# Performance work log

Measured on AMD Instinct MI355X. Metric: run time of the kernel, lower is better.

Reference implementation:

```python
import jax, jax.numpy as jnp
import numpy as np

L = 64          # lattice side
NSITES = L * L  # 4096
HALF = NSITES // 2
B = 16384
H = 128         # hidden width of s/t MLPs
SLOPE = 0.2     # tf.nn.leaky_relu default alpha

# checkerboard parity indices (static, evenodd = 0)
_coords = np.arange(NSITES)
_parity = (_coords // L + _coords % L) % 2
IDX_A = jnp.asarray(np.where(_parity == 0)[0], dtype=jnp.int32)  # [HALF]
IDX_B = jnp.asarray(np.where(_parity == 1)[0], dtype=jnp.int32)  # [HALF]


def setup_inputs() -> dict:
    key = jax.random.key(0)
    ks = jax.random.split(key, 8)
    scale = 0.05  # small init keeps exp(-s) well-behaved
    return {
        "z":    jax.random.normal(ks[0], (B, NSITES), dtype=jnp.float32),
        "s_W0": jax.random.normal(ks[1], (HALF, H), dtype=jnp.float32) * scale,
        "s_W1": jax.random.normal(ks[2], (H, H), dtype=jnp.float32) * scale,
        "s_W2": jax.random.normal(ks[3], (H, HALF), dtype=jnp.float32) * scale,
        "s_b2": jnp.zeros((HALF,), dtype=jnp.float32),
        "t_W0": jax.random.normal(ks[4], (HALF, H), dtype=jnp.float32) * scale,
        "t_W1": jax.random.normal(ks[5], (H, H), dtype=jnp.float32) * scale,
        "t_W2": jax.random.normal(ks[6], (H, HALF), dtype=jnp.float32) * scale,
        "t_b2": jnp.zeros((HALF,), dtype=jnp.float32),
    }


def _mlp(x, W0, W1, W2, b2):
    # Dense(no bias)+leaky_relu x2, then Dense(with bias), matching the keras stack
    h = jax.nn.leaky_relu(x @ W0, negative_slope=SLOPE)
    h = jax.nn.leaky_relu(h @ W1, negative_slope=SLOPE)
    return h @ W2 + b2


def reference(z, s_W0, s_W1, s_W2, s_b2, t_W0, t_W1, t_W2, t_b2):
    z_a = z[:, IDX_A]                       # [B, HALF] gather (even sites)
    z_b = z[:, IDX_B]                       # [B, HALF] gather (odd sites)
    s_out = _mlp(z_a, s_W0, s_W1, s_W2, s_b2)   # [B, HALF]
    t_a = _mlp(z_a, t_W0, t_W1, t_W2, t_b2)     # [B, HALF]
    s_a = jnp.exp(-s_out)
    f_b = (z_b - t_a) * s_a                 # affine coupling
    # scatter back (disjoint indices -> set is equivalent to scatter_nd add)
    f = jnp.zeros_like(z).at[:, IDX_A].set(z_a).at[:, IDX_B].set(f_b)
    d = jnp.sum(s_out, axis=1)              # logdetjacfwd: sum of s(z_a)
    return (f, d)
```

## Files before the change

kernel.cpp:

```cpp
#include <hip/hip_runtime.h>
#include <hip/hip_bf16.h>

#define BATCH  16384
#define SLOPE  0.2f
#define BM     32

typedef __attribute__((ext_vector_type(8))) short bf16x8;
typedef __attribute__((ext_vector_type(4))) float f32x4;
typedef __attribute__((ext_vector_type(4))) float fx4;
typedef __attribute__((ext_vector_type(2))) float fx2;

#define OFF_SW0T 0
#define OFF_TW0T 262144
#define OFF_SW1T 524288
#define OFF_TW1T 540672
#define OFF_SW2T 557056
#define OFF_TW2T 819200

__device__ __forceinline__ unsigned short f2bf(float f) {
    unsigned int u = __float_as_uint(f);
    u += 0x7FFFu + ((u >> 16) & 1u);
    return (unsigned short)(u >> 16);
}

__global__ void conv_w(const float* __restrict__ sW0, const float* __restrict__ sW1,
                       const float* __restrict__ sW2, const float* __restrict__ tW0,
                       const float* __restrict__ tW1, const float* __restrict__ tW2,
                       unsigned short* __restrict__ ws) {
    const int total = 262144 + 16384 + 262144;
    for (int i = blockIdx.x * blockDim.x + threadIdx.x; i < total;
         i += gridDim.x * blockDim.x) {
        if (i < 262144) {
            int k = i >> 7, n = i & 127;
            int ks = (k & ~63) | ((((k >> 3) & 7) ^ (n & 7)) << 3) | (k & 7);
            ws[OFF_SW0T + n * 2048 + ks] = f2bf(sW0[i]);
            ws[OFF_TW0T + n * 2048 + ks] = f2bf(tW0[i]);
        } else if (i < 262144 + 16384) {
            int j = i - 262144;
            int k = j >> 7, n = j & 127;
            ws[OFF_SW1T + n * 128 + k] = f2bf(sW1[j]);
            ws[OFF_TW1T + n * 128 + k] = f2bf(tW1[j]);
        } else {
            int j = i - (262144 + 16384);
            int k = j >> 11, n = j & 2047;
            int ks = ((((k >> 3) & 15) ^ (n & 7)) << 3) | (k & 7);
            ws[OFF_SW2T + n * 128 + ks] = f2bf(sW2[j]);
            ws[OFF_TW2T + n * 128 + ks] = f2bf(tW2[j]);
        }
    }
}

__global__ __launch_bounds__(256, 2) void coupling_main(
    const float* __restrict__ z,
    const float* __restrict__ s_b2,
    const float* __restrict__ t_b2,
    const unsigned short* __restrict__ ws,
    float* __restrict__ f_out,
    float* __restrict__ d_vec) {

    __shared__ __align__(16) unsigned char LDSbuf[73728];
    unsigned short* HA = (unsigned short*)(LDSbuf + 8192);
    unsigned short* HB = (unsigned short*)(LDSbuf + 24576);
    float* Dred = (float*)(LDSbuf + 65536);

    const int tid  = threadIdx.x;
    const int wave = tid >> 6;
    const int lane = tid & 63;
    const int l15  = lane & 15;
    const int l4   = lane >> 4;
    const int brow = blockIdx.x * BM;

    const char* wsb = (const char*)ws;
    const fx4* __restrict__ zf4 = (const fx4*)z;
    const fx2* __restrict__ zf2 = (const fx2*)z;
    fx2* __restrict__ ff2 = (fx2*)f_out;

    auto ldzTo = [&](fx4 (&zr)[4], int c) {
        #pragma unroll
        for (int q = 0; q < 4; ++q) {
            const int f = tid + 256 * q;
            const int row = f >> 5, col16 = f & 31;
            zr[q] = __builtin_nontemporal_load(
                zf4 + (size_t)(brow + row) * 1024 + c * 32 + col16);
        }
    };
    auto wrzFrom = [&](fx4 (&zr)[4], int b) {
        #pragma unroll
        for (int q = 0; q < 4; ++q) {
            const int f = tid + 256 * q;
            const int row = f >> 5, col16 = f & 31;
            const int par = (col16 >> 4) & 1;
            const float a0 = par ? zr[q].y : zr[q].x;
            const float a1 = par ? zr[q].w : zr[q].z;
            const unsigned int pk = (unsigned int)f2bf(a0) | ((unsigned int)f2bf(a1) << 16);
            *(unsigned int*)(LDSbuf + b * 4096 + row * 128 +
                             (((col16 >> 2) ^ (row & 7)) << 4) + (col16 & 3) * 4) = pk;
        }
    };
    auto stageW0 = [&](int b, int c) {
        #pragma unroll
        for (int jj = 0; jj < 8; ++jj) {
            const char* g = wsb + (size_t)(wave * 64 + jj * 8 + (lane >> 3)) * 4096
                            + c * 128 + (lane & 7) * 16;
            void* l = LDSbuf + 8192 + b * 32768 + (wave * 64 + jj * 8) * 128;
            __builtin_amdgcn_global_load_lds(
                (const __attribute__((address_space(1))) unsigned int*)g,
                (__attribute__((address_space(3))) unsigned int*)l, 16, 0, 0);
        }
    };

    f32x4 acc0[2][4] = {};
    auto cmp0 = [&](int cb) {
        const char* Az = (const char*)(LDSbuf + cb * 4096);
        const char* Wt = (const char*)(LDSbuf + 8192 + cb * 32768);
        bf16x8 af[2][2], wf[4][2];
        #pragma unroll
        for (int m = 0; m < 2; ++m)
            #pragma unroll
            for (int k2 = 0; k2 < 2; ++k2) {
                const int row = m * 16 + l15;
                af[m][k2] = *(const bf16x8*)(Az + row * 128 +
                              ((k2 * 64 + l4 * 16) ^ ((row & 7) << 4)));
            }
        #pragma unroll
        for (int n2 = 0; n2 < 4; ++n2)
            #pragma unroll
            for (int k2 = 0; k2 < 2; ++k2) {
                const int g = wave * 64 + n2 * 16 + l15;
                wf[n2][k2] = *(const bf16x8*)(Wt + g * 128 +
                               ((k2 * 64 + l4 * 16) ^ ((g & 7) << 4)));
            }
        #pragma unroll
        for (int n2 = 0; n2 < 4; ++n2)
            #pragma unroll
            for (int k2 = 0; k2 < 2; ++k2)
                #pragma unroll
                for (int m = 0; m < 2; ++m)
                    acc0[m][n2] = __builtin_amdgcn_mfma_f32_16x16x32_bf16(
                        af[m][k2], wf[n2][k2], acc0[m][n2], 0, 0, 0);
    };

    fx4 zA[4], zB[4];
    auto phase = [&](int p, int cb, fx4 (&zLd)[4], fx4 (&zWr)[4]) {
        if (p + 1 < 32) stageW0(cb ^ 1, p + 1);
        if (p + 2 < 32) ldzTo(zLd, p + 2);
        cmp0(cb);
        if (p + 1 < 32) wrzFrom(zWr, cb ^ 1);
        if (p + 2 < 32)
            asm volatile("s_waitcnt lgkmcnt(0) vmcnt(4)" ::: "memory");
        else
            asm volatile("s_waitcnt lgkmcnt(0) vmcnt(0)" ::: "memory");
        __builtin_amdgcn_s_barrier();
        __builtin_amdgcn_sched_barrier(0);
    };

    ldzTo(zB, 0);
    stageW0(0, 0);
    wrzFrom(zB, 0);
    ldzTo(zB, 1);
    asm volatile("s_waitcnt lgkmcnt(0) vmcnt(4)" ::: "memory");
    __builtin_amdgcn_s_barrier();
    __builtin_amdgcn_sched_barrier(0);

    #pragma unroll 1
    for (int gIt = 0; gIt < 16; ++gIt) {
        phase(2 * gIt,     0, zA, zB);
        phase(2 * gIt + 1, 1, zB, zA);
    }

    #pragma unroll
    for (int m = 0; m < 2; ++m)
        #pragma unroll
        for (int n2 = 0; n2 < 4; ++n2)
            #pragma unroll
            for (int r = 0; r < 4; ++r) {
                float v = acc0[m][n2][r];
                v = v > 0.0f ? v : SLOPE * v;
                const int row = m * 16 + l4 * 4 + r;
                const int col = wave * 64 + n2 * 16 + l15;
                HA[row * 256 + (col ^ ((row & 7) << 3))] = f2bf(v);
            }
    __syncthreads();

    f32x4 acc1[2][4] = {};
    const int net1 = wave >> 1;
    #pragma unroll
    for (int k4 = 0; k4 < 4; ++k4) {
        bf16x8 ahv[2];
        #pragma unroll
        for (int m = 0; m < 2; ++m) {
            const int row = m * 16 + l15;
            ahv[m] = *(const bf16x8*)&HA[row * 256 +
                       ((net1 * 128 + k4 * 32 + l4 * 8) ^ ((row & 7) << 3))];
        }
        #pragma unroll
        for (int n2 = 0; n2 < 4; ++n2) {
            const bf16x8 w = *(const bf16x8*)&ws[OFF_SW1T +
                (size_t)(wave * 64 + n2 * 16 + l15) * 128 + k4 * 32 + l4 * 8];
            #pragma unroll
            for (int m = 0; m < 2; ++m)
                acc1[m][n2] = __builtin_amdgcn_mfma_f32_16x16x32_bf16(
                    ahv[m], w, acc1[m][n2], 0, 0, 0);
        }
    }
    __syncthreads();
    #pragma unroll
    for (int m = 0; m < 2; ++m)
        #pragma unroll
        for (int n2 = 0; n2 < 4; ++n2)
            #pragma unroll
            for (int r = 0; r < 4; ++r) {
                float v = acc1[m][n2][r];
                v = v > 0.0f ? v : SLOPE * v;
                const int row = m * 16 + l4 * 4 + r;
                const int col = wave * 64 + n2 * 16 + l15;
                HB[row * 256 + (col ^ ((row & 7) << 3))] = f2bf(v);
            }
    __syncthreads();

    const int par = wave >> 1;

    bf16x8 ahs[2][4], aht[2][4];
    #pragma unroll
    for (int m = 0; m < 2; ++m)
        #pragma unroll
        for (int k4 = 0; k4 < 4; ++k4) {
            const int row = m * 16 + l15;
            const int kc = k4 * 32 + l4 * 8;
            ahs[m][k4] = *(const bf16x8*)&HB[row * 256 + (kc ^ ((row & 7) << 3))];
            aht[m][k4] = *(const bf16x8*)&HB[row * 256 + ((128 + kc) ^ ((row & 7) << 3))];
        }
    __syncthreads();

    auto stageW2 = [&](int b, int c2) {
        #pragma unroll
        for (int jj = 0; jj < 8; ++jj) {
            const int r  = wave * 32 + jj * 4 + (lane >> 4);
            const int pr = c2 * 64 + (r & 63);
            const char* g = wsb + (size_t)((r >> 6) ? OFF_TW2T : OFF_SW2T) * 2
                            + (size_t)pr * 256 + (lane & 15) * 16;
            void* l = LDSbuf + b * 32768 + (wave * 32 + jj * 4) * 256;
            __builtin_amdgcn_global_load_lds(
                (const __attribute__((address_space(1))) unsigned int*)g,
                (__attribute__((address_space(3))) unsigned int*)l, 16, 0, 0);
        }
    };

    float dsum[2][4] = {};

    fx2 zvA[2][4], zvB[2][4];
    float sbA, tbA, sbB, tbB;
    auto ldzEp = [&](fx2 (&zv)[2][4], float& sb, float& tb, int c2) {
        const int j = c2 * 64 + wave * 16 + l15;
        sb = s_b2[j];
        tb = t_b2[j];
        #pragma unroll
        for (int m = 0; m < 2; ++m)
            #pragma unroll
            for (int r = 0; r < 4; ++r)
                zv[m][r] = __builtin_nontemporal_load(
                    &zf2[(size_t)(brow + m * 16 + l4 * 4 + r) * 2048 + j]);
    };

    auto l2body = [&](fx2 (&zv)[2][4], float sb, float tb, int c2, int cb) {
        bf16x8 wfs[4], wft[4];
        #pragma unroll
        for (int k4 = 0; k4 < 4; ++k4) {
            const int rs = wave * 16 + l15;
            const int rt = 64 + wave * 16 + l15;
            const int kc = k4 * 64 + l4 * 16;
            wfs[k4] = *(const bf16x8*)(LDSbuf + cb * 32768 + rs * 256 + (kc ^ ((rs & 7) << 4)));
            wft[k4] = *(const bf16x8*)(LDSbuf + cb * 32768 + rt * 256 + (kc ^ ((rt & 7) << 4)));
        }
        f32x4 acc2[2][2] = {};
        #pragma unroll
        for (int k4 = 0; k4 < 4; ++k4)
            #pragma unroll
            for (int m = 0; m < 2; ++m) {
                acc2[0][m] = __builtin_amdgcn_mfma_f32_16x16x32_bf16(
                    ahs[m][k4], wfs[k4], acc2[0][m], 0, 0, 0);
                acc2[1][m] = __builtin_amdgcn_mfma_f32_16x16x32_bf16(
                    aht[m][k4], wft[k4], acc2[1][m], 0, 0, 0);
            }
        const int j = c2 * 64 + wave * 16 + l15;
        #pragma unroll
        for (int m = 0; m < 2; ++m)
            #pragma unroll
            for (int r = 0; r < 4; ++r) {
                const float sv = acc2[0][m][r] + sb;
                const float tv = acc2[1][m][r] + tb;
                const fx2 zp = zv[m][r];
                const float za = par ? zp.y : zp.x;
                const float zb = par ? zp.x : zp.y;
                const float fb = (zb - tv) * __expf(-sv);
                fx2 fv;
                if (par) { fv.x = fb; fv.y = za; }
                else     { fv.x = za; fv.y = fb; }
                __builtin_nontemporal_store(fv,
                    &ff2[(size_t)(brow + m * 16 + l4 * 4 + r) * 2048 + j]);
                dsum[m][r] += sv;
            }
    };

    stageW2(0, 0);
    ldzEp(zvA, sbA, tbA, 0);
    __syncthreads();

    #pragma unroll 1
    for (int it = 0; it < 16; ++it) {
        {
            const int c2 = 2 * it;
            ldzEp(zvB, sbB, tbB, c2 + 1);
            stageW2(1, c2 + 1);
            l2body(zvA, sbA, tbA, c2, 0);
            __syncthreads();
        }
        {
            const int c2 = 2 * it + 1;
            if (c2 < 31) {
                ldzEp(zvA, sbA, tbA, c2 + 1);
                stageW2(0, c2 + 1);
            }
            l2body(zvB, sbB, tbB, c2, 1);
            __syncthreads();
        }
    }

    #pragma unroll
    for (int m = 0; m < 2; ++m)
        #pragma unroll
        for (int r = 0; r < 4; ++r) {
            float v = dsum[m][r];
            v += __shfl_xor(v, 1);
            v += __shfl_xor(v, 2);
            v += __shfl_xor(v, 4);
            v += __shfl_xor(v, 8);
            if (l15 == 0) Dred[wave * 32 + m * 16 + l4 * 4 + r] = v;
        }
    __syncthreads();
    if (tid < BM)
        d_vec[brow + tid] = Dred[tid] + Dred[32 + tid] + Dred[64 + tid] + Dred[96 + tid];
}

extern "C" void kernel_launch(void* const* d_in, const int* in_sizes, int n_in,
                              void* d_out, int out_size, void* d_ws, size_t ws_size,
                              hipStream_t stream) {
    const float* z   = (const float*)d_in[0];
    const float* sW0 = (const float*)d_in[1];
    const float* sW1 = (const float*)d_in[2];
    const float* sW2 = (const float*)d_in[3];
    const float* sb2 = (const float*)d_in[4];
    const float* tW0 = (const float*)d_in[5];
    const float* tW1 = (const float*)d_in[6];
    const float* tW2 = (const float*)d_in[7];
    const float* tb2 = (const float*)d_in[8];

    float* fout = (float*)d_out;
    float* dvec = fout + (size_t)BATCH * 4096;
    unsigned short* ws = (unsigned short*)d_ws;

    hipLaunchKernelGGL(conv_w, dim3(512), dim3(256), 0, stream,
                       sW0, sW1, sW2, tW0, tW1, tW2, ws);
    hipLaunchKernelGGL(coupling_main, dim3(BATCH / BM), dim3(256), 0, stream,
                       z, sb2, tb2, ws, fout, dvec);
}
```

Before: 188.5 us.

## Replace barriers with per-wave vmcnt waits so each wave stages its own W2 slice

Each wave now stages into LDS only the W2 rows it later reads itself, for both the s and t nets. This lets the layer-2 loop drop its __syncthreads and depend on fine-grained s_waitcnt vmcnt counts instead. In the layer-0 pipeline, the vmcnt wait moves ahead of the MFMA compute, leaving only an lgkmcnt wait at the barrier. The aim is to cut barrier stalls and let loads overlap compute more. The hand-tuned vmcnt counts are fragile: if they are wrong, or if ordering within a wave fails to cover the LDS reads, results can be stale.

```diff
diff --git a/kernel.cpp b/kernel.cpp
--- a/kernel.cpp
+++ b/kernel.cpp
@@ -144,12 +144,15 @@
     auto phase = [&](int p, int cb, fx4 (&zLd)[4], fx4 (&zWr)[4]) {
         if (p + 1 < 32) stageW0(cb ^ 1, p + 1);
         if (p + 2 < 32) ldzTo(zLd, p + 2);
+        if (p <= 29)
+            asm volatile("s_waitcnt vmcnt(16)" ::: "memory");
+        else if (p == 30)
+            asm volatile("s_waitcnt vmcnt(12)" ::: "memory");
+        else
+            asm volatile("s_waitcnt vmcnt(0)" ::: "memory");
         cmp0(cb);
         if (p + 1 < 32) wrzFrom(zWr, cb ^ 1);
-        if (p + 2 < 32)
-            asm volatile("s_waitcnt lgkmcnt(0) vmcnt(4)" ::: "memory");
-        else
-            asm volatile("s_waitcnt lgkmcnt(0) vmcnt(0)" ::: "memory");
+        asm volatile("s_waitcnt lgkmcnt(0)" ::: "memory");
         __builtin_amdgcn_s_barrier();
         __builtin_amdgcn_sched_barrier(0);
     };
@@ -158,7 +161,7 @@
     stageW0(0, 0);
     wrzFrom(zB, 0);
     ldzTo(zB, 1);
-    asm volatile("s_waitcnt lgkmcnt(0) vmcnt(4)" ::: "memory");
+    asm volatile("s_waitcnt lgkmcnt(0)" ::: "memory");
     __builtin_amdgcn_s_barrier();
     __builtin_amdgcn_sched_barrier(0);
 
@@ -235,11 +238,12 @@
     auto stageW2 = [&](int b, int c2) {
         #pragma unroll
         for (int jj = 0; jj < 8; ++jj) {
-            const int r  = wave * 32 + jj * 4 + (lane >> 4);
-            const int pr = c2 * 64 + (r & 63);
-            const char* g = wsb + (size_t)((r >> 6) ? OFF_TW2T : OFF_SW2T) * 2
+            const int net  = jj >> 2;
+            const int rloc = wave * 16 + (jj & 3) * 4 + (lane >> 4);
+            const int pr   = c2 * 64 + rloc;
+            const char* g = wsb + (size_t)(net ? OFF_TW2T : OFF_SW2T) * 2
                             + (size_t)pr * 256 + (lane & 15) * 16;
-            void* l = LDSbuf + b * 32768 + (wave * 32 + jj * 4) * 256;
+            void* l = LDSbuf + b * 32768 + (net * 64 + wave * 16 + (jj & 3) * 4) * 256;
             __builtin_amdgcn_global_load_lds(
                 (const __attribute__((address_space(1))) unsigned int*)g,
                 (__attribute__((address_space(3))) unsigned int*)l, 16, 0, 0);
@@ -304,25 +308,29 @@
 
     stageW2(0, 0);
     ldzEp(zvA, sbA, tbA, 0);
-    __syncthreads();
 
     #pragma unroll 1
     for (int it = 0; it < 16; ++it) {
         {
             const int c2 = 2 * it;
+            stageW2(1, c2 + 1);
             ldzEp(zvB, sbB, tbB, c2 + 1);
-            stageW2(1, c2 + 1);
+            if (c2 == 0)
+                asm volatile("s_waitcnt vmcnt(28)" ::: "memory");
+            else
+                asm volatile("s_waitcnt vmcnt(36)" ::: "memory");
             l2body(zvA, sbA, tbA, c2, 0);
-            __syncthreads();
         }
         {
             const int c2 = 2 * it + 1;
             if (c2 < 31) {
+                stageW2(0, c2 + 1);
                 ldzEp(zvA, sbA, tbA, c2 + 1);
-                stageW2(0, c2 + 1);
+                asm volatile("s_waitcnt vmcnt(36)" ::: "memory");
+            } else {
+                asm volatile("s_waitcnt vmcnt(18)" ::: "memory");
             }
             l2body(zvB, sbB, tbB, c2, 1);
-            __syncthreads();
         }
     }
 
```

Result: slower. 207.9 us (+10.3%).
